# Kernel tuning notes

Hardware: AMD Instinct MI355X
Metric: run time of the kernel (lower is better)

## Reference

```python
import jax, jax.numpy as jnp
import numpy as np

N_NODES = 50000
N_EDGES = 800000
D_NODE = 64
D_EDGE = 64


def setup_inputs() -> dict:
    key = jax.random.key(0)
    ks = jax.random.split(key, 6)
    node_scalars = jax.random.normal(ks[0], (N_NODES, D_NODE), dtype=jnp.float32)
    edge_feats = jax.random.normal(ks[1], (N_EDGES, D_EDGE), dtype=jnp.float32)
    src_idxs = jax.random.randint(ks[2], (N_EDGES,), 0, N_NODES, dtype=jnp.int32)
    dst_idxs = jax.random.randint(ks[3], (N_EDGES,), 0, N_NODES, dtype=jnp.int32)
    in_dim = 2 * D_NODE + D_EDGE  # 192
    # He-ish init for the MLP weights
    W1 = jax.random.normal(ks[4], (in_dim, D_EDGE), dtype=jnp.float32) / np.sqrt(in_dim)
    b1 = jnp.zeros((D_EDGE,), dtype=jnp.float32)
    W2 = jax.random.normal(ks[5], (D_EDGE, D_EDGE), dtype=jnp.float32) / np.sqrt(D_EDGE)
    b2 = jnp.zeros((D_EDGE,), dtype=jnp.float32)
    ln_gamma = jnp.ones((D_EDGE,), dtype=jnp.float32)
    ln_beta = jnp.zeros((D_EDGE,), dtype=jnp.float32)
    return {
        "node_scalars": node_scalars,
        "edge_feats": edge_feats,
        "src_idxs": src_idxs,
        "dst_idxs": dst_idxs,
        "W1": W1,
        "b1": b1,
        "W2": W2,
        "b2": b2,
        "ln_gamma": ln_gamma,
        "ln_beta": ln_beta,
    }


def _layer_norm(x, gamma, beta, eps=1e-5):
    mu = jnp.mean(x, axis=-1, keepdims=True)
    var = jnp.mean(jnp.square(x - mu), axis=-1, keepdims=True)
    return (x - mu) * jax.lax.rsqrt(var + eps) * gamma + beta


def reference(node_scalars, edge_feats, src_idxs, dst_idxs, W1, b1, W2, b2, ln_gamma, ln_beta):
    # gather endpoint node features per edge and concat with edge feats -> [E, 2*Dn + De]
    mlp_in = jnp.concatenate(
        [node_scalars[src_idxs], node_scalars[dst_idxs], edge_feats], axis=-1
    )
    h = jax.nn.silu(mlp_in @ W1 + b1)
    h = jax.nn.silu(h @ W2 + b2)
    return _layer_norm(edge_feats + h, ln_gamma, ln_beta)
```

## Files before the change

kernel.cpp:

```cpp
#include <hip/hip_runtime.h>

#define NE 800000
#define D  64
#define K1 192

typedef __bf16 bf16x8 __attribute__((ext_vector_type(8)));
typedef float  f32x4  __attribute__((ext_vector_type(4)));

__global__ void prep_weights(const float* __restrict__ W1,
                             const float* __restrict__ W2,
                             __bf16* __restrict__ ws) {
  int i = blockIdx.x * 256 + threadIdx.x;
  if (i < K1 * D) {
    int k = i >> 6, n = i & 63;
    ws[n * K1 + k] = (__bf16)W1[i];
  } else {
    int j = i - K1 * D;
    int k = j >> 6, n = j & 63;
    ws[K1 * D + n * D + k] = (__bf16)W2[j];
  }
}

__device__ __forceinline__ void wave_lds_fence() {
  __asm__ volatile("s_waitcnt lgkmcnt(0)" ::: "memory");
}

template <bool USE_WS>
__global__ __launch_bounds__(256, 4)
void edge_kernel(const float* __restrict__ nodes, const float* __restrict__ ef,
                 const int* __restrict__ srci, const int* __restrict__ dsti,
                 const float* __restrict__ W1, const float* __restrict__ b1,
                 const float* __restrict__ W2, const float* __restrict__ b2,
                 const float* __restrict__ gmm, const float* __restrict__ bta,
                 const __bf16* __restrict__ wsw, float* __restrict__ out) {
  __shared__ __align__(16) __bf16 w1t[64 * 200];
  __shared__ __align__(16) __bf16 hbuf[4][16 * 72];
  __shared__ float sb1[64], sb2[64], sg[64], sbt[64];

  const int tid = threadIdx.x;
  const int wave = tid >> 6, lane = tid & 63;
  const int quad = lane >> 4, m16 = lane & 15;

  if (USE_WS) {
    const uint2* s1 = (const uint2*)wsw;
    for (int c = tid; c < 3072; c += 256) {
      int n = c / 48, kc = c - n * 48;
      *(uint2*)&w1t[n * 200 + kc * 4] = s1[c];
    }
  } else {
    for (int i = tid; i < K1 * D; i += 256) {
      int k = i >> 6, n = i & 63;
      w1t[n * 200 + k] = (__bf16)W1[i];
    }
  }
  if (tid < 64)       sb1[tid]       = b1[tid];
  else if (tid < 128) sb2[tid - 64]  = b2[tid - 64];
  else if (tid < 192) sg[tid - 128]  = gmm[tid - 128];
  else                sbt[tid - 192] = bta[tid - 192];

  bf16x8 w2f[2][4];
  if (USE_WS) {
    const __bf16* w2t = wsw + K1 * D;
    #pragma unroll
    for (int ki = 0; ki < 2; ++ki)
      #pragma unroll
      for (int nt = 0; nt < 4; ++nt)
        w2f[ki][nt] = *(const bf16x8*)&w2t[(nt * 16 + m16) * 64 + ki * 32 + quad * 8];
  } else {
    #pragma unroll
    for (int ki = 0; ki < 2; ++ki)
      #pragma unroll
      for (int nt = 0; nt < 4; ++nt) {
        const int n = nt * 16 + m16;
        #pragma unroll
        for (int j = 0; j < 8; ++j)
          w2f[ki][nt][j] = (__bf16)W2[(ki * 32 + quad * 8 + j) * 64 + n];
      }
  }
  __syncthreads();

  __bf16* hw = hbuf[wave];

  #pragma unroll 1
  for (int t = 0; t < 4; ++t) {
    const int base = blockIdx.x * 256 + wave * 64 + t * 16;
    const int eRow = base + m16;
    const int s = srci[eRow], d = dsti[eRow];
    const float* r0 = nodes + (size_t)s * D;
    const float* r1 = nodes + (size_t)d * D;
    const float* r2 = ef + (size_t)eRow * D;

    f32x4 acc[4] = {};
    #pragma unroll
    for (int ki = 0; ki < 6; ++ki) {
      const float* p;
      if (ki < 2)      p = r0 + ki * 32 + quad * 8;
      else if (ki < 4) p = r1 + (ki - 2) * 32 + quad * 8;
      else             p = r2 + (ki - 4) * 32 + quad * 8;
      f32x4 lo = *(const f32x4*)p;
      f32x4 hi = *(const f32x4*)(p + 4);
      bf16x8 a;
      a[0] = (__bf16)lo[0]; a[1] = (__bf16)lo[1];
      a[2] = (__bf16)lo[2]; a[3] = (__bf16)lo[3];
      a[4] = (__bf16)hi[0]; a[5] = (__bf16)hi[1];
      a[6] = (__bf16)hi[2]; a[7] = (__bf16)hi[3];
      const int wk = ki * 32 + quad * 8;
      #pragma unroll
      for (int nt = 0; nt < 4; ++nt) {
        bf16x8 bf = *(const bf16x8*)&w1t[(nt * 16 + m16) * 200 + wk];
        acc[nt] = __builtin_amdgcn_mfma_f32_16x16x32_bf16(a, bf, acc[nt], 0, 0, 0);
      }
    }

    #pragma unroll
    for (int nt = 0; nt < 4; ++nt) {
      const int c = nt * 16 + m16;
      const float bb = sb1[c];
      #pragma unroll
      for (int r = 0; r < 4; ++r) {
        float x = acc[nt][r] + bb;
        float sv = x * __builtin_amdgcn_rcpf(1.f + __expf(-x));
        hw[(quad * 4 + r) * 72 + c] = (__bf16)sv;
      }
    }
    wave_lds_fence();

    f32x4 acc2[4] = {};
    #pragma unroll
    for (int ki = 0; ki < 2; ++ki) {
      bf16x8 a = *(const bf16x8*)&hw[m16 * 72 + ki * 32 + quad * 8];
      #pragma unroll
      for (int nt = 0; nt < 4; ++nt)
        acc2[nt] = __builtin_amdgcn_mfma_f32_16x16x32_bf16(a, w2f[ki][nt], acc2[nt], 0, 0, 0);
    }
    wave_lds_fence();

    #pragma unroll
    for (int r = 0; r < 4; ++r) {
      const int row = quad * 4 + r;
      const size_t eo = (size_t)(base + row) * D;
      float x[4];
      float sum = 0.f;
      #pragma unroll
      for (int nt = 0; nt < 4; ++nt) {
        const int c = nt * 16 + m16;
        float h = acc2[nt][r] + sb2[c];
        h = h * __builtin_amdgcn_rcpf(1.f + __expf(-h));
        x[nt] = ef[eo + c] + h;
        sum += x[nt];
      }
      float sq = x[0] * x[0] + x[1] * x[1] + x[2] * x[2] + x[3] * x[3];
      #pragma unroll
      for (int off = 1; off < 16; off <<= 1) {
        sum += __shfl_xor(sum, off);
        sq  += __shfl_xor(sq, off);
      }
      const float mean = sum * (1.f / 64.f);
      const float var  = sq * (1.f / 64.f) - mean * mean;
      const float rstd = rsqrtf(var + 1e-5f);
      #pragma unroll
      for (int nt = 0; nt < 4; ++nt) {
        const int c = nt * 16 + m16;
        out[eo + c] = (x[nt] - mean) * rstd * sg[c] + sbt[c];
      }
    }
  }
}

extern "C" void kernel_launch(void* const* d_in, const int* in_sizes, int n_in,
                              void* d_out, int out_size, void* d_ws, size_t ws_size,
                              hipStream_t stream) {
  const float* nodes = (const float*)d_in[0];
  const float* ef    = (const float*)d_in[1];
  const int*   srci  = (const int*)d_in[2];
  const int*   dsti  = (const int*)d_in[3];
  const float* W1    = (const float*)d_in[4];
  const float* b1    = (const float*)d_in[5];
  const float* W2    = (const float*)d_in[6];
  const float* b2    = (const float*)d_in[7];
  const float* gmm   = (const float*)d_in[8];
  const float* bta   = (const float*)d_in[9];
  float* out = (float*)d_out;

  const int blocks = NE / 256;
  if (ws_size >= (size_t)(K1 * D + D * D) * 2) {
    prep_weights<<<64, 256, 0, stream>>>(W1, W2, (__bf16*)d_ws);
    edge_kernel<true><<<blocks, 256, 0, stream>>>(
        nodes, ef, srci, dsti, W1, b1, W2, b2, gmm, bta,
        (const __bf16*)d_ws, out);
  } else {
    edge_kernel<false><<<blocks, 256, 0, stream>>>(
        nodes, ef, srci, dsti, W1, b1, W2, b2, gmm, bta, nullptr, out);
  }
}
```

Before: 471.0 us.

## Stage gathered inputs and outputs through LDS for vectorized coalesced access

Each wave now gathers the src, dst and edge rows with 16-byte loads where 16 lanes cover one row. It converts them to bf16 and writes them into a per-wave LDS tile, and the first MFMA reads its A fragments from that tile. The layer-norm result is also staged in LDS so the output is written with full-row 16-byte vector stores instead of scattered 4-byte stores. The residual now reads edge features from the bf16 LDS copy rather than fp32 global memory, which saves a reload but lowers residual precision. The larger LDS footprint lowers the occupancy hint from 4 to 3 blocks.

After: 403.0 us. 14.5% less time.

```diff
diff --git a/kernel.cpp b/kernel.cpp
--- a/kernel.cpp
+++ b/kernel.cpp
@@ -3,9 +3,11 @@
 #define NE 800000
 #define D  64
 #define K1 192
-
-typedef __bf16 bf16x8 __attribute__((ext_vector_type(8)));
-typedef float  f32x4  __attribute__((ext_vector_type(4)));
+#define AST 200
+
+typedef __bf16 bf16x4v __attribute__((ext_vector_type(4)));
+typedef __bf16 bf16x8  __attribute__((ext_vector_type(8)));
+typedef float  f32x4   __attribute__((ext_vector_type(4)));
 
 __global__ void prep_weights(const float* __restrict__ W1,
                              const float* __restrict__ W2,
@@ -25,16 +27,20 @@
   __asm__ volatile("s_waitcnt lgkmcnt(0)" ::: "memory");
 }
 
+__device__ __forceinline__ float silu(float x) {
+  return x * __builtin_amdgcn_rcpf(1.f + __expf(-x));
+}
+
 template <bool USE_WS>
-__global__ __launch_bounds__(256, 4)
+__global__ __launch_bounds__(256, 3)
 void edge_kernel(const float* __restrict__ nodes, const float* __restrict__ ef,
                  const int* __restrict__ srci, const int* __restrict__ dsti,
                  const float* __restrict__ W1, const float* __restrict__ b1,
                  const float* __restrict__ W2, const float* __restrict__ b2,
                  const float* __restrict__ gmm, const float* __restrict__ bta,
                  const __bf16* __restrict__ wsw, float* __restrict__ out) {
-  __shared__ __align__(16) __bf16 w1t[64 * 200];
-  __shared__ __align__(16) __bf16 hbuf[4][16 * 72];
+  __shared__ __align__(16) __bf16 w1t[64 * AST];
+  __shared__ __align__(16) __bf16 atile_all[4][16 * AST];
   __shared__ float sb1[64], sb2[64], sg[64], sbt[64];
 
   const int tid = threadIdx.x;
@@ -45,12 +51,12 @@
     const uint2* s1 = (const uint2*)wsw;
     for (int c = tid; c < 3072; c += 256) {
       int n = c / 48, kc = c - n * 48;
-      *(uint2*)&w1t[n * 200 + kc * 4] = s1[c];
+      *(uint2*)&w1t[n * AST + kc * 4] = s1[c];
     }
   } else {
     for (int i = tid; i < K1 * D; i += 256) {
       int k = i >> 6, n = i & 63;
-      w1t[n * 200 + k] = (__bf16)W1[i];
+      w1t[n * AST + k] = (__bf16)W1[i];
     }
   }
   if (tid < 64)       sb1[tid]       = b1[tid];
@@ -79,36 +85,44 @@
   }
   __syncthreads();
 
-  __bf16* hw = hbuf[wave];
+  __bf16* At = atile_all[wave];
+  float*  Af = (float*)At;
 
   #pragma unroll 1
   for (int t = 0; t < 4; ++t) {
     const int base = blockIdx.x * 256 + wave * 64 + t * 16;
-    const int eRow = base + m16;
-    const int s = srci[eRow], d = dsti[eRow];
-    const float* r0 = nodes + (size_t)s * D;
-    const float* r1 = nodes + (size_t)d * D;
-    const float* r2 = ef + (size_t)eRow * D;
+
+    int si[4], di[4];
+    #pragma unroll
+    for (int i = 0; i < 4; ++i) {
+      si[i] = srci[base + i * 4 + quad];
+      di[i] = dsti[base + i * 4 + quad];
+    }
+    #pragma unroll
+    for (int i = 0; i < 4; ++i) {
+      const int row = i * 4 + quad;
+      f32x4 sv = *(const f32x4*)(nodes + (size_t)si[i] * D + m16 * 4);
+      f32x4 dv = *(const f32x4*)(nodes + (size_t)di[i] * D + m16 * 4);
+      f32x4 ev = *(const f32x4*)(ef + (size_t)(base + row) * D + m16 * 4);
+      bf16x4v sb, db, eb;
+      #pragma unroll
+      for (int j = 0; j < 4; ++j) {
+        sb[j] = (__bf16)sv[j]; db[j] = (__bf16)dv[j]; eb[j] = (__bf16)ev[j];
+      }
+      *(bf16x4v*)&At[row * AST +       m16 * 4] = sb;
+      *(bf16x4v*)&At[row * AST +  64 + m16 * 4] = db;
+      *(bf16x4v*)&At[row * AST + 128 + m16 * 4] = eb;
+    }
+    wave_lds_fence();
 
     f32x4 acc[4] = {};
     #pragma unroll
     for (int ki = 0; ki < 6; ++ki) {
-      const float* p;
-      if (ki < 2)      p = r0 + ki * 32 + quad * 8;
-      else if (ki < 4) p = r1 + (ki - 2) * 32 + quad * 8;
-      else             p = r2 + (ki - 4) * 32 + quad * 8;
-      f32x4 lo = *(const f32x4*)p;
-      f32x4 hi = *(const f32x4*)(p + 4);
-      bf16x8 a;
-      a[0] = (__bf16)lo[0]; a[1] = (__bf16)lo[1];
-      a[2] = (__bf16)lo[2]; a[3] = (__bf16)lo[3];
-      a[4] = (__bf16)hi[0]; a[5] = (__bf16)hi[1];
-      a[6] = (__bf16)hi[2]; a[7] = (__bf16)hi[3];
-      const int wk = ki * 32 + quad * 8;
-      #pragma unroll
-      for (int nt = 0; nt < 4; ++nt) {
-        bf16x8 bf = *(const bf16x8*)&w1t[(nt * 16 + m16) * 200 + wk];
-        acc[nt] = __builtin_amdgcn_mfma_f32_16x16x32_bf16(a, bf, acc[nt], 0, 0, 0);
+      bf16x8 a = *(const bf16x8*)&At[m16 * AST + ki * 32 + quad * 8];
+      #pragma unroll
+      for (int nt = 0; nt < 4; ++nt) {
+        bf16x8 bfv = *(const bf16x8*)&w1t[(nt * 16 + m16) * AST + ki * 32 + quad * 8];
+        acc[nt] = __builtin_amdgcn_mfma_f32_16x16x32_bf16(a, bfv, acc[nt], 0, 0, 0);
       }
     }
 
@@ -117,36 +131,31 @@
       const int c = nt * 16 + m16;
       const float bb = sb1[c];
       #pragma unroll
-      for (int r = 0; r < 4; ++r) {
-        float x = acc[nt][r] + bb;
-        float sv = x * __builtin_amdgcn_rcpf(1.f + __expf(-x));
-        hw[(quad * 4 + r) * 72 + c] = (__bf16)sv;
-      }
+      for (int r = 0; r < 4; ++r)
+        At[(quad * 4 + r) * AST + c] = (__bf16)silu(acc[nt][r] + bb);
     }
     wave_lds_fence();
 
     f32x4 acc2[4] = {};
     #pragma unroll
     for (int ki = 0; ki < 2; ++ki) {
-      bf16x8 a = *(const bf16x8*)&hw[m16 * 72 + ki * 32 + quad * 8];
+      bf16x8 a = *(const bf16x8*)&At[m16 * AST + ki * 32 + quad * 8];
       #pragma unroll
       for (int nt = 0; nt < 4; ++nt)
         acc2[nt] = __builtin_amdgcn_mfma_f32_16x16x32_bf16(a, w2f[ki][nt], acc2[nt], 0, 0, 0);
     }
-    wave_lds_fence();
 
     #pragma unroll
     for (int r = 0; r < 4; ++r) {
       const int row = quad * 4 + r;
-      const size_t eo = (size_t)(base + row) * D;
       float x[4];
       float sum = 0.f;
       #pragma unroll
       for (int nt = 0; nt < 4; ++nt) {
         const int c = nt * 16 + m16;
-        float h = acc2[nt][r] + sb2[c];
-        h = h * __builtin_amdgcn_rcpf(1.f + __expf(-h));
-        x[nt] = ef[eo + c] + h;
+        float h = silu(acc2[nt][r] + sb2[c]);
+        float efv = (float)At[row * AST + 128 + c];
+        x[nt] = efv + h;
         sum += x[nt];
       }
       float sq = x[0] * x[0] + x[1] * x[1] + x[2] * x[2] + x[3] * x[3];
@@ -161,9 +170,18 @@
       #pragma unroll
       for (int nt = 0; nt < 4; ++nt) {
         const int c = nt * 16 + m16;
-        out[eo + c] = (x[nt] - mean) * rstd * sg[c] + sbt[c];
-      }
-    }
+        Af[row * (AST / 2) + c] = (x[nt] - mean) * rstd * sg[c] + sbt[c];
+      }
+    }
+    wave_lds_fence();
+
+    #pragma unroll
+    for (int i = 0; i < 4; ++i) {
+      const int row = i * 4 + quad;
+      f32x4 ov = *(const f32x4*)&Af[row * (AST / 2) + m16 * 4];
+      *(f32x4*)(out + (size_t)(base + row) * D + m16 * 4) = ov;
+    }
+    wave_lds_fence();
   }
 }
 
```
